# Performance work log

Hardware: AMD Instinct MI355X
Metric: run time of the kernel (lower is better)

## Reference

```python
import jax, jax.numpy as jnp
import numpy as np

N_NODES = 100000
N_EDGES = 1600000
IN_F, HID_F, OUT_F = 64, 64, 64


def setup_inputs() -> dict:
    key = jax.random.key(0)
    ks = jax.random.split(key, 9)
    return {
        "x": jax.random.normal(ks[0], (N_NODES, IN_F), dtype=jnp.float32),
        "src": jax.random.randint(ks[1], (N_EDGES,), 0, N_NODES, dtype=jnp.int64),
        "dst": jax.random.randint(ks[2], (N_EDGES,), 0, N_NODES, dtype=jnp.int64),
        "W_self1": jax.random.normal(ks[3], (IN_F, HID_F), dtype=jnp.float32) * (1.0 / np.sqrt(IN_F)),
        "W_neigh1": jax.random.normal(ks[4], (IN_F, HID_F), dtype=jnp.float32) * (1.0 / np.sqrt(IN_F)),
        "b1": jnp.zeros((HID_F,), dtype=jnp.float32),
        "W_self2": jax.random.normal(ks[5], (HID_F, OUT_F), dtype=jnp.float32) * (1.0 / np.sqrt(HID_F)),
        "W_neigh2": jax.random.normal(ks[6], (HID_F, OUT_F), dtype=jnp.float32) * (1.0 / np.sqrt(HID_F)),
        "b2": jnp.zeros((OUT_F,), dtype=jnp.float32),
    }


def reference(x, src, dst, W_self1, W_neigh1, b1, W_self2, W_neigh2, b2):
    N = x.shape[0]
    # in-degree per destination node; zero-in-degree nodes get zero aggregate (DGL semantics)
    deg = jax.ops.segment_sum(jnp.ones(dst.shape, dtype=x.dtype), dst, num_segments=N)
    inv_deg = jnp.where(deg > 0, 1.0 / jnp.maximum(deg, 1.0), 0.0)[:, None]  # [N,1]

    def sage_conv(h, W_s, W_n, b):
        # mean over in-neighbors: gather src feats, segment-sum at dst, normalize
        agg = jax.ops.segment_sum(h[src], dst, num_segments=N) * inv_deg  # [N,F]
        return h @ W_s + agg @ W_n + b

    h = jax.nn.relu(sage_conv(x, W_self1, W_neigh1, b1))
    return sage_conv(h, W_self2, W_neigh2, b2)
```

## Files before the change

### kernel.cpp

```cpp
#include <hip/hip_runtime.h>

#define N_NODES 100000
#define N_EDGES 1600000
#define NBKT 392
#define BKT_SHIFT 8
#define BKT_MASK 255
#define DL_SHIFT 17
#define SRC_MASK 0x1FFFF
#define NT_TILES 6250
#define CNT_BLOCKS 256
#define CVT_BLOCKS 6250

typedef __attribute__((ext_vector_type(8))) short short8;
typedef __attribute__((ext_vector_type(4))) float float4v;

__device__ __forceinline__ unsigned short f2bf(float f) {
  unsigned u = __float_as_uint(f);
  return (unsigned short)((u + 0x7fffu + ((u >> 16) & 1u)) >> 16);
}
__device__ __forceinline__ float bflo(unsigned d) { return __uint_as_float(d << 16); }
__device__ __forceinline__ float bfhi(unsigned d) { return __uint_as_float(d & 0xffff0000u); }

__device__ __forceinline__ void acc_add(float a[8], uint4 v) {
  a[0] += bflo(v.x); a[1] += bfhi(v.x);
  a[2] += bflo(v.y); a[3] += bfhi(v.y);
  a[4] += bflo(v.z); a[5] += bfhi(v.z);
  a[6] += bflo(v.w); a[7] += bfhi(v.w);
}
__device__ __forceinline__ void acc_fma(float a[8], uint4 v, float m) {
  a[0] = fmaf(m, bflo(v.x), a[0]); a[1] = fmaf(m, bfhi(v.x), a[1]);
  a[2] = fmaf(m, bflo(v.y), a[2]); a[3] = fmaf(m, bfhi(v.y), a[3]);
  a[4] = fmaf(m, bflo(v.z), a[4]); a[5] = fmaf(m, bfhi(v.z), a[5]);
  a[6] = fmaf(m, bflo(v.w), a[6]); a[7] = fmaf(m, bfhi(v.w), a[7]);
}


__global__ void k_prep_count(const float* __restrict__ in, unsigned short* __restrict__ outb,
                             const float* __restrict__ W0, const float* __restrict__ W1,
                             const float* __restrict__ W2, const float* __restrict__ W3,
                             unsigned short* __restrict__ F,
                             const int* __restrict__ dst, int* __restrict__ blkCnt) {
  __shared__ int hist[NBKT];
  const int bid = blockIdx.x;
  if (bid < CNT_BLOCKS) {
    for (int t = threadIdx.x; t < NBKT; t += 256) hist[t] = 0;
    __syncthreads();
    const int e0 = bid * (N_EDGES / CNT_BLOCKS);
    const int e1 = e0 + (N_EDGES / CNT_BLOCKS);
    for (int e = e0 + threadIdx.x; e < e1; e += 256)
      atomicAdd(&hist[dst[e] >> BKT_SHIFT], 1);
    __syncthreads();
    for (int t = threadIdx.x; t < NBKT; t += 256)
      blkCnt[t * CNT_BLOCKS + bid] = hist[t];
    return;
  }
  if (bid < CNT_BLOCKS + 4) {
    if (threadIdx.x >= 64) return;
    const int wsel = bid - CNT_BLOCKS;
    const float* W = (wsel == 0) ? W0 : (wsel == 1) ? W1 : (wsel == 2) ? W2 : W3;
    unsigned short* out = F + wsel * 4096;
    int lane = threadIdx.x;
    int col = lane & 15, kr = lane >> 4;
    #pragma unroll
    for (int kc = 0; kc < 2; kc++)
      #pragma unroll
      for (int nt = 0; nt < 4; nt++) {
        unsigned d[4];
        #pragma unroll
        for (int jj = 0; jj < 4; jj++) {
          float w0 = W[(kc * 32 + kr * 8 + 2 * jj)     * 64 + nt * 16 + col];
          float w1 = W[(kc * 32 + kr * 8 + 2 * jj + 1) * 64 + nt * 16 + col];
          d[jj] = ((unsigned)f2bf(w1) << 16) | f2bf(w0);
        }
        uint4* p = (uint4*)(out + ((kc * 4 + nt) * 64 + lane) * 8);
        *p = make_uint4(d[0], d[1], d[2], d[3]);
      }
    return;
  }
  int i = (bid - CNT_BLOCKS - 4) * 256 + threadIdx.x;
  float4 v = ((const float4*)in)[i];
  unsigned d0 = ((unsigned)f2bf(v.y) << 16) | f2bf(v.x);
  unsigned d1 = ((unsigned)f2bf(v.w) << 16) | f2bf(v.z);
  ((uint2*)outb)[i] = make_uint2(d0, d1);
}


__global__ void kA_scan1(int* __restrict__ blkCnt, int* __restrict__ bktTot) {
  const int b = blockIdx.x;
  const int tid = threadIdx.x, lane = tid & 63, w = tid >> 6;
  int v = blkCnt[b * CNT_BLOCKS + tid];
  int inc = v;
  #pragma unroll
  for (int d = 1; d < 64; d <<= 1) { int y = __shfl_up(inc, d); if (lane >= d) inc += y; }
  __shared__ int wtot[4];
  if (lane == 63) wtot[w] = inc;
  __syncthreads();
  int base = 0;
  for (int j = 0; j < w; j++) base += wtot[j];
  blkCnt[b * CNT_BLOCKS + tid] = base + inc - v;
  if (tid == CNT_BLOCKS - 1) bktTot[b] = base + inc;
}


__global__ void kA_scatter(const int* __restrict__ src, const int* __restrict__ dst,
                           const int* __restrict__ blkCnt, const int* __restrict__ bktTot,
                           int* __restrict__ bktStart, int* __restrict__ binned) {
  __shared__ int ps[NBKT];
  __shared__ int curb[NBKT];
  const int tid = threadIdx.x;
  if (tid < 64) {
    int running = 0;
    for (int base = 0; base < NBKT; base += 64) {
      int i = base + tid;
      int v = (i < NBKT) ? bktTot[i] : 0;
      int inc = v;
      #pragma unroll
      for (int d = 1; d < 64; d <<= 1) { int y = __shfl_up(inc, d); if (tid >= d) inc += y; }
      if (i < NBKT) ps[i] = running + inc - v;
      running += __shfl(inc, 63);
    }
  }
  __syncthreads();
  for (int t = tid; t < NBKT; t += 256)
    curb[t] = ps[t] + blkCnt[t * CNT_BLOCKS + blockIdx.x];
  if (blockIdx.x == 0)
    for (int t = tid; t < NBKT; t += 256) bktStart[t] = ps[t];
  __syncthreads();
  const int e0 = blockIdx.x * (N_EDGES / CNT_BLOCKS);
  const int e1 = e0 + (N_EDGES / CNT_BLOCKS);
  for (int e = e0 + tid; e < e1; e += 256) {
    int d = dst[e];
    int s = src[e];
    int b = d >> BKT_SHIFT;
    int p = atomicAdd(&curb[b], 1);
    binned[p] = s | ((d & BKT_MASK) << DL_SHIFT);
  }
}


__global__ __launch_bounds__(512)
void k_sort(const int* __restrict__ binned, const int* __restrict__ bktStart,
            const int* __restrict__ bktTot,
            int* __restrict__ off, int* __restrict__ esrc) {
  const int b = blockIdx.x;
  const int tid = threadIdx.x, lane = tid & 63, w = tid >> 6;
  __shared__ int cnt[256];
  __shared__ int pos[256];
  __shared__ int wtot[4];
  if (tid < 256) cnt[tid] = 0;
  __syncthreads();
  const int s0 = bktStart[b], ne = bktTot[b];
  for (int i = tid; i < ne; i += 512)
    atomicAdd(&cnt[binned[s0 + i] >> DL_SHIFT], 1);
  __syncthreads();
  if (tid < 256) {
    int c = cnt[tid];
    int inc = c;
    #pragma unroll
    for (int d = 1; d < 64; d <<= 1) { int y = __shfl_up(inc, d); if (lane >= d) inc += y; }
    if (lane == 63) wtot[w] = inc;
    __syncthreads();
    int base = s0;
    for (int j = 0; j < w; j++) base += wtot[j];
    int ex = base + inc - c;
    pos[tid] = ex;
    int n0 = (b << BKT_SHIFT) + tid;
    if (n0 < N_NODES) off[n0] = ex;
    if (n0 == N_NODES - 1) off[N_NODES] = N_EDGES;
  } else {
    __syncthreads();
  }
  __syncthreads();
  for (int i = tid; i < ne; i += 512) {
    int pe = binned[s0 + i];
    int p = atomicAdd(&pos[pe >> DL_SHIFT], 1);
    esrc[p] = pe & SRC_MASK;
  }
}


template <bool RELU, bool OUT_BF>
__global__ void k_fused(const unsigned short* __restrict__ featb,
                        const int* __restrict__ off, const int* __restrict__ esrc,
                        const unsigned short* __restrict__ wfS,
                        const unsigned short* __restrict__ wfN,
                        const float* __restrict__ bias,
                        float* __restrict__ outf, unsigned short* __restrict__ outb) {
  __shared__ unsigned short aggl[4][16 * 64];
  const int tid = threadIdx.x;
  const int lane = tid & 63;
  const int wslot = tid >> 6;
  const int t = (blockIdx.x * blockDim.x + tid) >> 6;
  if (t >= NT_TILES) return;

  unsigned short* lw = &aggl[wslot][0];
  const int n = lane >> 3;
  const int h = lane & 7;

  #pragma unroll
  for (int half = 0; half < 2; ++half) {
    const int row = half * 8 + n;
    const int node = t * 16 + row;
    const int o0 = off[node];
    const int o1 = off[node + 1];
    float a[8];
    #pragma unroll
    for (int q = 0; q < 8; q++) a[q] = 0.f;

    int i = o0;
    for (; i + 8 <= o1; i += 8) {
      int s0 = esrc[i],     s1 = esrc[i + 1], s2 = esrc[i + 2], s3 = esrc[i + 3];
      int s4 = esrc[i + 4], s5 = esrc[i + 5], s6 = esrc[i + 6], s7 = esrc[i + 7];
      uint4 v0 = *(const uint4*)(featb + s0 * 64 + h * 8);
      uint4 v1 = *(const uint4*)(featb + s1 * 64 + h * 8);
      uint4 v2 = *(const uint4*)(featb + s2 * 64 + h * 8);
      uint4 v3 = *(const uint4*)(featb + s3 * 64 + h * 8);
      uint4 v4 = *(const uint4*)(featb + s4 * 64 + h * 8);
      uint4 v5 = *(const uint4*)(featb + s5 * 64 + h * 8);
      uint4 v6 = *(const uint4*)(featb + s6 * 64 + h * 8);
      uint4 v7 = *(const uint4*)(featb + s7 * 64 + h * 8);
      acc_add(a, v0); acc_add(a, v1); acc_add(a, v2); acc_add(a, v3);
      acc_add(a, v4); acc_add(a, v5); acc_add(a, v6); acc_add(a, v7);
    }
    if (i + 4 <= o1) {
      int s0 = esrc[i], s1 = esrc[i + 1], s2 = esrc[i + 2], s3 = esrc[i + 3];
      uint4 v0 = *(const uint4*)(featb + s0 * 64 + h * 8);
      uint4 v1 = *(const uint4*)(featb + s1 * 64 + h * 8);
      uint4 v2 = *(const uint4*)(featb + s2 * 64 + h * 8);
      uint4 v3 = *(const uint4*)(featb + s3 * 64 + h * 8);
      acc_add(a, v0); acc_add(a, v1); acc_add(a, v2); acc_add(a, v3);
      i += 4;
    }
    if (i < o1) {
      int last = o1 - 1;
      int e1 = min(i + 1, last), e2 = min(i + 2, last);
      float m1 = (i + 1 < o1) ? 1.f : 0.f;
      float m2 = (i + 2 < o1) ? 1.f : 0.f;
      int s0 = esrc[i], s1 = esrc[e1], s2 = esrc[e2];
      uint4 v0 = *(const uint4*)(featb + s0 * 64 + h * 8);
      uint4 v1 = *(const uint4*)(featb + s1 * 64 + h * 8);
      uint4 v2 = *(const uint4*)(featb + s2 * 64 + h * 8);
      acc_add(a, v0); acc_fma(a, v1, m1); acc_fma(a, v2, m2);
    }

    const int dg = o1 - o0;
    const float inv = (dg > 0) ? (1.0f / (float)dg) : 0.f;
    unsigned d0 = ((unsigned)f2bf(a[1] * inv) << 16) | f2bf(a[0] * inv);
    unsigned d1 = ((unsigned)f2bf(a[3] * inv) << 16) | f2bf(a[2] * inv);
    unsigned d2 = ((unsigned)f2bf(a[5] * inv) << 16) | f2bf(a[4] * inv);
    unsigned d3 = ((unsigned)f2bf(a[7] * inv) << 16) | f2bf(a[6] * inv);
    *(uint4*)(lw + row * 64 + ((h ^ (row & 7)) << 3)) = make_uint4(d0, d1, d2, d3);
  }

  __builtin_amdgcn_wave_barrier();
  asm volatile("" ::: "memory");

  const int col = lane & 15, rr = lane >> 4;
  const int m = t * 16 + col;
  short8 as0 = *(const short8*)(featb + m * 64 + rr * 8);
  short8 as1 = *(const short8*)(featb + m * 64 + 32 + rr * 8);
  short8 aa0 = *(const short8*)(lw + col * 64 + ((rr ^ (col & 7)) << 3));
  short8 aa1 = *(const short8*)(lw + col * 64 + (((rr + 4) ^ (col & 7)) << 3));

  #pragma unroll
  for (int nt = 0; nt < 4; nt++) {
    short8 bs0 = *(const short8*)(wfS + ((0 * 4 + nt) * 64 + lane) * 8);
    short8 bs1 = *(const short8*)(wfS + ((1 * 4 + nt) * 64 + lane) * 8);
    short8 bn0 = *(const short8*)(wfN + ((0 * 4 + nt) * 64 + lane) * 8);
    short8 bn1 = *(const short8*)(wfN + ((1 * 4 + nt) * 64 + lane) * 8);
    float bvn = bias[nt * 16 + col];
    float4v cfr = {bvn, bvn, bvn, bvn};
    cfr = __builtin_amdgcn_mfma_f32_16x16x32_bf16(as0, bs0, cfr, 0, 0, 0);
    cfr = __builtin_amdgcn_mfma_f32_16x16x32_bf16(as1, bs1, cfr, 0, 0, 0);
    cfr = __builtin_amdgcn_mfma_f32_16x16x32_bf16(aa0, bn0, cfr, 0, 0, 0);
    cfr = __builtin_amdgcn_mfma_f32_16x16x32_bf16(aa1, bn1, cfr, 0, 0, 0);
    #pragma unroll
    for (int r2 = 0; r2 < 4; r2++) {
      int row = t * 16 + rr * 4 + r2;
      float v = cfr[r2];
      if (RELU) v = fmaxf(v, 0.f);
      if (OUT_BF) outb[row * 64 + nt * 16 + col] = f2bf(v);
      else        outf[row * 64 + nt * 16 + col] = v;
    }
  }
}


extern "C" void kernel_launch(void* const* d_in, const int* in_sizes, int n_in,
                              void* d_out, int out_size, void* d_ws, size_t ws_size,
                              hipStream_t stream) {
  const float* x   = (const float*)d_in[0];
  const int*   src = (const int*)d_in[1];
  const int*   dst = (const int*)d_in[2];
  const float* Ws1 = (const float*)d_in[3];
  const float* Wn1 = (const float*)d_in[4];
  const float* b1  = (const float*)d_in[5];
  const float* Ws2 = (const float*)d_in[6];
  const float* Wn2 = (const float*)d_in[7];
  const float* b2  = (const float*)d_in[8];

  char* ws = (char*)d_ws;
  int*            blkCnt   = (int*)(ws + 0);
  int*            bktTot   = (int*)(ws + 401408);
  int*            bktStart = (int*)(ws + 403008);
  unsigned short* wf       = (unsigned short*)(ws + 404608);
  int*            off      = (int*)(ws + 437376);
  int*            binned   = (int*)(ws + 837440);
  int*            esrc     = (int*)(ws + 7237440);
  unsigned short* xbf      = (unsigned short*)(ws + 13637440);
  unsigned short* hbf      = (unsigned short*)(ws + 26437440);

  k_prep_count<<<CNT_BLOCKS + 4 + CVT_BLOCKS, 256, 0, stream>>>(
      x, xbf, Ws1, Wn1, Ws2, Wn2, wf, dst, blkCnt);
  kA_scan1<<<NBKT, 256, 0, stream>>>(blkCnt, bktTot);
  kA_scatter<<<CNT_BLOCKS, 256, 0, stream>>>(src, dst, blkCnt, bktTot, bktStart, binned);
  k_sort<<<NBKT, 512, 0, stream>>>(binned, bktStart, bktTot, off, esrc);

  k_fused<true, true><<<1563, 256, 0, stream>>>(xbf, off, esrc, wf + 0 * 4096,
                                                wf + 1 * 4096, b1, nullptr, hbf);
  k_fused<false, false><<<1563, 256, 0, stream>>>(hbf, off, esrc, wf + 2 * 4096,
                                                  wf + 3 * 4096, b2, (float*)d_out, nullptr);
}
```

Before: 238.8 us.

## Fuse bucket scan into scatter and CSR sort into first SAGE layer

Removes the separate scan and sort kernels. Each scatter block now recomputes the bucket totals and its own prefix from the count matrix, and the first layer's fused kernel builds its per-bucket CSR in LDS and aggregates from there, while also writing off/esrc for layer two. Buckets shrink to 128 nodes, and the bf16 conversion now does four elements per thread. This cuts launches and global round trips of the edge lists, at the cost of redundant per-block row sums. It also caps per-bucket edges at ESRC_CAP, which assumes a fairly uniform in-degree distribution.

After: 217.6 us. 8.9% less time.

```diff
diff --git a/kernel.cpp b/kernel.cpp
--- a/kernel.cpp
+++ b/kernel.cpp
@@ -2,14 +2,16 @@
 
 #define N_NODES 100000
 #define N_EDGES 1600000
-#define NBKT 392
-#define BKT_SHIFT 8
-#define BKT_MASK 255
+#define BKT 128
+#define NBKT 782
+#define BKT_SHIFT 7
+#define BKT_MASK 127
 #define DL_SHIFT 17
 #define SRC_MASK 0x1FFFF
 #define NT_TILES 6250
-#define CNT_BLOCKS 256
-#define CVT_BLOCKS 6250
+#define CNT_BLOCKS 128
+#define CVT_BLOCKS 1563
+#define ESRC_CAP 3072
 
 typedef __attribute__((ext_vector_type(8))) short short8;
 typedef __attribute__((ext_vector_type(4))) float float4v;
@@ -77,42 +79,47 @@
       }
     return;
   }
-  int i = (bid - CNT_BLOCKS - 4) * 256 + threadIdx.x;
-  float4 v = ((const float4*)in)[i];
-  unsigned d0 = ((unsigned)f2bf(v.y) << 16) | f2bf(v.x);
-  unsigned d1 = ((unsigned)f2bf(v.w) << 16) | f2bf(v.z);
-  ((uint2*)outb)[i] = make_uint2(d0, d1);
-}
-
-
-__global__ void kA_scan1(int* __restrict__ blkCnt, int* __restrict__ bktTot) {
-  const int b = blockIdx.x;
-  const int tid = threadIdx.x, lane = tid & 63, w = tid >> 6;
-  int v = blkCnt[b * CNT_BLOCKS + tid];
-  int inc = v;
-  #pragma unroll
-  for (int d = 1; d < 64; d <<= 1) { int y = __shfl_up(inc, d); if (lane >= d) inc += y; }
-  __shared__ int wtot[4];
-  if (lane == 63) wtot[w] = inc;
-  __syncthreads();
-  int base = 0;
-  for (int j = 0; j < w; j++) base += wtot[j];
-  blkCnt[b * CNT_BLOCKS + tid] = base + inc - v;
-  if (tid == CNT_BLOCKS - 1) bktTot[b] = base + inc;
-}
-
-
-__global__ void kA_scatter(const int* __restrict__ src, const int* __restrict__ dst,
-                           const int* __restrict__ blkCnt, const int* __restrict__ bktTot,
-                           int* __restrict__ bktStart, int* __restrict__ binned) {
+  const int base = (bid - CNT_BLOCKS - 4) * 1024 + threadIdx.x;
+  #pragma unroll
+  for (int j = 0; j < 4; j++) {
+    int i = base + j * 256;
+    if (i < 1600000) {
+      float4 v = ((const float4*)in)[i];
+      unsigned d0 = ((unsigned)f2bf(v.y) << 16) | f2bf(v.x);
+      unsigned d1 = ((unsigned)f2bf(v.w) << 16) | f2bf(v.z);
+      ((uint2*)outb)[i] = make_uint2(d0, d1);
+    }
+  }
+}
+
+
+__global__ __launch_bounds__(512)
+void k_scatter(const int* __restrict__ src, const int* __restrict__ dst,
+               const int* __restrict__ blkCnt, int* __restrict__ bktStart,
+               int* __restrict__ bktTot, int* __restrict__ binned) {
+  __shared__ int totsh[NBKT];
   __shared__ int ps[NBKT];
   __shared__ int curb[NBKT];
   const int tid = threadIdx.x;
+  const int bid = blockIdx.x;
+  for (int t = tid; t < NBKT; t += 512) {
+    const int* row = blkCnt + t * CNT_BLOCKS;
+    int tot = 0, part = 0;
+    #pragma unroll 4
+    for (int i = 0; i < CNT_BLOCKS; i++) {
+      int v = row[i];
+      tot += v;
+      if (i < bid) part += v;
+    }
+    totsh[t] = tot;
+    curb[t] = part;
+  }
+  __syncthreads();
   if (tid < 64) {
     int running = 0;
     for (int base = 0; base < NBKT; base += 64) {
       int i = base + tid;
-      int v = (i < NBKT) ? bktTot[i] : 0;
+      int v = (i < NBKT) ? totsh[i] : 0;
       int inc = v;
       #pragma unroll
       for (int d = 1; d < 64; d <<= 1) { int y = __shfl_up(inc, d); if (tid >= d) inc += y; }
@@ -121,129 +128,104 @@
     }
   }
   __syncthreads();
-  for (int t = tid; t < NBKT; t += 256)
-    curb[t] = ps[t] + blkCnt[t * CNT_BLOCKS + blockIdx.x];
-  if (blockIdx.x == 0)
-    for (int t = tid; t < NBKT; t += 256) bktStart[t] = ps[t];
-  __syncthreads();
-  const int e0 = blockIdx.x * (N_EDGES / CNT_BLOCKS);
+  for (int t = tid; t < NBKT; t += 512) curb[t] += ps[t];
+  if (bid == 0)
+    for (int t = tid; t < NBKT; t += 512) { bktStart[t] = ps[t]; bktTot[t] = totsh[t]; }
+  __syncthreads();
+  const int e0 = bid * (N_EDGES / CNT_BLOCKS);
   const int e1 = e0 + (N_EDGES / CNT_BLOCKS);
-  for (int e = e0 + tid; e < e1; e += 256) {
+  for (int e = e0 + tid; e < e1; e += 512) {
     int d = dst[e];
     int s = src[e];
-    int b = d >> BKT_SHIFT;
-    int p = atomicAdd(&curb[b], 1);
+    int p = atomicAdd(&curb[d >> BKT_SHIFT], 1);
     binned[p] = s | ((d & BKT_MASK) << DL_SHIFT);
   }
 }
 
 
 __global__ __launch_bounds__(512)
-void k_sort(const int* __restrict__ binned, const int* __restrict__ bktStart,
-            const int* __restrict__ bktTot,
-            int* __restrict__ off, int* __restrict__ esrc) {
+void k_fused1(const unsigned short* __restrict__ featb, const int* __restrict__ binned,
+              const int* __restrict__ bktStart, const int* __restrict__ bktTot,
+              const unsigned short* __restrict__ wfS, const unsigned short* __restrict__ wfN,
+              const float* __restrict__ bias,
+              unsigned short* __restrict__ outb,
+              int* __restrict__ off, int* __restrict__ esrc) {
+  __shared__ int cnt[BKT];
+  __shared__ int st[BKT];
+  __shared__ int pos[BKT];
+  __shared__ int wtot[2];
+  __shared__ int esrc_l[ESRC_CAP];
+  __shared__ unsigned short aggl[8][16 * 64];
   const int b = blockIdx.x;
-  const int tid = threadIdx.x, lane = tid & 63, w = tid >> 6;
-  __shared__ int cnt[256];
-  __shared__ int pos[256];
-  __shared__ int wtot[4];
-  if (tid < 256) cnt[tid] = 0;
+  const int tid = threadIdx.x, lane = tid & 63;
+  const int wv = tid >> 6;
+
+  if (tid < BKT) cnt[tid] = 0;
   __syncthreads();
   const int s0 = bktStart[b], ne = bktTot[b];
   for (int i = tid; i < ne; i += 512)
     atomicAdd(&cnt[binned[s0 + i] >> DL_SHIFT], 1);
   __syncthreads();
-  if (tid < 256) {
-    int c = cnt[tid];
-    int inc = c;
+  int c = 0, inc = 0;
+  if (tid < BKT) {
+    c = cnt[tid]; inc = c;
     #pragma unroll
     for (int d = 1; d < 64; d <<= 1) { int y = __shfl_up(inc, d); if (lane >= d) inc += y; }
-    if (lane == 63) wtot[w] = inc;
-    __syncthreads();
-    int base = s0;
-    for (int j = 0; j < w; j++) base += wtot[j];
-    int ex = base + inc - c;
-    pos[tid] = ex;
+    if (lane == 63) wtot[tid >> 6] = inc;
+  }
+  __syncthreads();
+  if (tid < BKT) {
+    int ex = inc - c + ((tid >= 64) ? wtot[0] : 0);
+    st[tid] = ex; pos[tid] = ex;
     int n0 = (b << BKT_SHIFT) + tid;
-    if (n0 < N_NODES) off[n0] = ex;
+    if (n0 < N_NODES) off[n0] = s0 + ex;
     if (n0 == N_NODES - 1) off[N_NODES] = N_EDGES;
-  } else {
-    __syncthreads();
   }
   __syncthreads();
   for (int i = tid; i < ne; i += 512) {
     int pe = binned[s0 + i];
     int p = atomicAdd(&pos[pe >> DL_SHIFT], 1);
-    esrc[p] = pe & SRC_MASK;
-  }
-}
-
-
-template <bool RELU, bool OUT_BF>
-__global__ void k_fused(const unsigned short* __restrict__ featb,
-                        const int* __restrict__ off, const int* __restrict__ esrc,
-                        const unsigned short* __restrict__ wfS,
-                        const unsigned short* __restrict__ wfN,
-                        const float* __restrict__ bias,
-                        float* __restrict__ outf, unsigned short* __restrict__ outb) {
-  __shared__ unsigned short aggl[4][16 * 64];
-  const int tid = threadIdx.x;
-  const int lane = tid & 63;
-  const int wslot = tid >> 6;
-  const int t = (blockIdx.x * blockDim.x + tid) >> 6;
-  if (t >= NT_TILES) return;
-
-  unsigned short* lw = &aggl[wslot][0];
+    if (p < ESRC_CAP) esrc_l[p] = pe & SRC_MASK;
+  }
+  __syncthreads();
+  for (int i = tid; i < ne; i += 512) esrc[s0 + i] = esrc_l[i];
+
+  unsigned short* lw = &aggl[wv][0];
   const int n = lane >> 3;
   const int h = lane & 7;
 
   #pragma unroll
   for (int half = 0; half < 2; ++half) {
     const int row = half * 8 + n;
-    const int node = t * 16 + row;
-    const int o0 = off[node];
-    const int o1 = off[node + 1];
+    const int lnode = wv * 16 + row;
+    const int o0 = st[lnode];
+    const int dg = cnt[lnode];
+    const int o1 = o0 + dg;
     float a[8];
     #pragma unroll
     for (int q = 0; q < 8; q++) a[q] = 0.f;
 
     int i = o0;
-    for (; i + 8 <= o1; i += 8) {
-      int s0 = esrc[i],     s1 = esrc[i + 1], s2 = esrc[i + 2], s3 = esrc[i + 3];
-      int s4 = esrc[i + 4], s5 = esrc[i + 5], s6 = esrc[i + 6], s7 = esrc[i + 7];
-      uint4 v0 = *(const uint4*)(featb + s0 * 64 + h * 8);
-      uint4 v1 = *(const uint4*)(featb + s1 * 64 + h * 8);
-      uint4 v2 = *(const uint4*)(featb + s2 * 64 + h * 8);
-      uint4 v3 = *(const uint4*)(featb + s3 * 64 + h * 8);
-      uint4 v4 = *(const uint4*)(featb + s4 * 64 + h * 8);
-      uint4 v5 = *(const uint4*)(featb + s5 * 64 + h * 8);
-      uint4 v6 = *(const uint4*)(featb + s6 * 64 + h * 8);
-      uint4 v7 = *(const uint4*)(featb + s7 * 64 + h * 8);
+    for (; i + 4 <= o1; i += 4) {
+      int s0e = esrc_l[i], s1e = esrc_l[i + 1], s2e = esrc_l[i + 2], s3e = esrc_l[i + 3];
+      uint4 v0 = *(const uint4*)(featb + s0e * 64 + h * 8);
+      uint4 v1 = *(const uint4*)(featb + s1e * 64 + h * 8);
+      uint4 v2 = *(const uint4*)(featb + s2e * 64 + h * 8);
+      uint4 v3 = *(const uint4*)(featb + s3e * 64 + h * 8);
       acc_add(a, v0); acc_add(a, v1); acc_add(a, v2); acc_add(a, v3);
-      acc_add(a, v4); acc_add(a, v5); acc_add(a, v6); acc_add(a, v7);
-    }
-    if (i + 4 <= o1) {
-      int s0 = esrc[i], s1 = esrc[i + 1], s2 = esrc[i + 2], s3 = esrc[i + 3];
-      uint4 v0 = *(const uint4*)(featb + s0 * 64 + h * 8);
-      uint4 v1 = *(const uint4*)(featb + s1 * 64 + h * 8);
-      uint4 v2 = *(const uint4*)(featb + s2 * 64 + h * 8);
-      uint4 v3 = *(const uint4*)(featb + s3 * 64 + h * 8);
-      acc_add(a, v0); acc_add(a, v1); acc_add(a, v2); acc_add(a, v3);
-      i += 4;
     }
     if (i < o1) {
       int last = o1 - 1;
       int e1 = min(i + 1, last), e2 = min(i + 2, last);
       float m1 = (i + 1 < o1) ? 1.f : 0.f;
       float m2 = (i + 2 < o1) ? 1.f : 0.f;
-      int s0 = esrc[i], s1 = esrc[e1], s2 = esrc[e2];
-      uint4 v0 = *(const uint4*)(featb + s0 * 64 + h * 8);
-      uint4 v1 = *(const uint4*)(featb + s1 * 64 + h * 8);
-      uint4 v2 = *(const uint4*)(featb + s2 * 64 + h * 8);
+      int s0e = esrc_l[i], s1e = esrc_l[e1], s2e = esrc_l[e2];
+      uint4 v0 = *(const uint4*)(featb + s0e * 64 + h * 8);
+      uint4 v1 = *(const uint4*)(featb + s1e * 64 + h * 8);
+      uint4 v2 = *(const uint4*)(featb + s2e * 64 + h * 8);
       acc_add(a, v0); acc_fma(a, v1, m1); acc_fma(a, v2, m2);
     }
 
-    const int dg = o1 - o0;
     const float inv = (dg > 0) ? (1.0f / (float)dg) : 0.f;
     unsigned d0 = ((unsigned)f2bf(a[1] * inv) << 16) | f2bf(a[0] * inv);
     unsigned d1 = ((unsigned)f2bf(a[3] * inv) << 16) | f2bf(a[2] * inv);
@@ -255,8 +237,10 @@
   __builtin_amdgcn_wave_barrier();
   asm volatile("" ::: "memory");
 
+  const int tbase = (b << BKT_SHIFT) + wv * 16;
+  if (tbase >= N_NODES) return;
   const int col = lane & 15, rr = lane >> 4;
-  const int m = t * 16 + col;
+  const int m = tbase + col;
   short8 as0 = *(const short8*)(featb + m * 64 + rr * 8);
   short8 as1 = *(const short8*)(featb + m * 64 + 32 + rr * 8);
   short8 aa0 = *(const short8*)(lw + col * 64 + ((rr ^ (col & 7)) << 3));
@@ -276,11 +260,96 @@
     cfr = __builtin_amdgcn_mfma_f32_16x16x32_bf16(aa1, bn1, cfr, 0, 0, 0);
     #pragma unroll
     for (int r2 = 0; r2 < 4; r2++) {
+      int row = tbase + rr * 4 + r2;
+      float v = fmaxf(cfr[r2], 0.f);
+      outb[row * 64 + nt * 16 + col] = f2bf(v);
+    }
+  }
+}
+
+
+__global__ void k_fused2(const unsigned short* __restrict__ featb,
+                         const int* __restrict__ off, const int* __restrict__ esrc,
+                         const unsigned short* __restrict__ wfS,
+                         const unsigned short* __restrict__ wfN,
+                         const float* __restrict__ bias, float* __restrict__ outf) {
+  __shared__ unsigned short aggl[4][16 * 64];
+  const int tid = threadIdx.x;
+  const int lane = tid & 63;
+  const int wslot = tid >> 6;
+  const int t = (blockIdx.x * blockDim.x + tid) >> 6;
+  if (t >= NT_TILES) return;
+
+  unsigned short* lw = &aggl[wslot][0];
+  const int n = lane >> 3;
+  const int h = lane & 7;
+
+  #pragma unroll
+  for (int half = 0; half < 2; ++half) {
+    const int row = half * 8 + n;
+    const int node = t * 16 + row;
+    const int o0 = off[node];
+    const int o1 = off[node + 1];
+    float a[8];
+    #pragma unroll
+    for (int q = 0; q < 8; q++) a[q] = 0.f;
+
+    int i = o0;
+    for (; i + 4 <= o1; i += 4) {
+      int s0 = esrc[i], s1 = esrc[i + 1], s2 = esrc[i + 2], s3 = esrc[i + 3];
+      uint4 v0 = *(const uint4*)(featb + s0 * 64 + h * 8);
+      uint4 v1 = *(const uint4*)(featb + s1 * 64 + h * 8);
+      uint4 v2 = *(const uint4*)(featb + s2 * 64 + h * 8);
+      uint4 v3 = *(const uint4*)(featb + s3 * 64 + h * 8);
+      acc_add(a, v0); acc_add(a, v1); acc_add(a, v2); acc_add(a, v3);
+    }
+    if (i < o1) {
+      int last = o1 - 1;
+      int e1 = min(i + 1, last), e2 = min(i + 2, last);
+      float m1 = (i + 1 < o1) ? 1.f : 0.f;
+      float m2 = (i + 2 < o1) ? 1.f : 0.f;
+      int s0 = esrc[i], s1 = esrc[e1], s2 = esrc[e2];
+      uint4 v0 = *(const uint4*)(featb + s0 * 64 + h * 8);
+      uint4 v1 = *(const uint4*)(featb + s1 * 64 + h * 8);
+      uint4 v2 = *(const uint4*)(featb + s2 * 64 + h * 8);
+      acc_add(a, v0); acc_fma(a, v1, m1); acc_fma(a, v2, m2);
+    }
+
+    const int dg = o1 - o0;
+    const float inv = (dg > 0) ? (1.0f / (float)dg) : 0.f;
+    unsigned d0 = ((unsigned)f2bf(a[1] * inv) << 16) | f2bf(a[0] * inv);
+    unsigned d1 = ((unsigned)f2bf(a[3] * inv) << 16) | f2bf(a[2] * inv);
+    unsigned d2 = ((unsigned)f2bf(a[5] * inv) << 16) | f2bf(a[4] * inv);
+    unsigned d3 = ((unsigned)f2bf(a[7] * inv) << 16) | f2bf(a[6] * inv);
+    *(uint4*)(lw + row * 64 + ((h ^ (row & 7)) << 3)) = make_uint4(d0, d1, d2, d3);
+  }
+
+  __builtin_amdgcn_wave_barrier();
+  asm volatile("" ::: "memory");
+
+  const int col = lane & 15, rr = lane >> 4;
+  const int m = t * 16 + col;
+  short8 as0 = *(const short8*)(featb + m * 64 + rr * 8);
+  short8 as1 = *(const short8*)(featb + m * 64 + 32 + rr * 8);
+  short8 aa0 = *(const short8*)(lw + col * 64 + ((rr ^ (col & 7)) << 3));
+  short8 aa1 = *(const short8*)(lw + col * 64 + (((rr + 4) ^ (col & 7)) << 3));
+
+  #pragma unroll
+  for (int nt = 0; nt < 4; nt++) {
+    short8 bs0 = *(const short8*)(wfS + ((0 * 4 + nt) * 64 + lane) * 8);
+    short8 bs1 = *(const short8*)(wfS + ((1 * 4 + nt) * 64 + lane) * 8);
+    short8 bn0 = *(const short8*)(wfN + ((0 * 4 + nt) * 64 + lane) * 8);
+    short8 bn1 = *(const short8*)(wfN + ((1 * 4 + nt) * 64 + lane) * 8);
+    float bvn = bias[nt * 16 + col];
+    float4v cfr = {bvn, bvn, bvn, bvn};
+    cfr = __builtin_amdgcn_mfma_f32_16x16x32_bf16(as0, bs0, cfr, 0, 0, 0);
+    cfr = __builtin_amdgcn_mfma_f32_16x16x32_bf16(as1, bs1, cfr, 0, 0, 0);
+    cfr = __builtin_amdgcn_mfma_f32_16x16x32_bf16(aa0, bn0, cfr, 0, 0, 0);
+    cfr = __builtin_amdgcn_mfma_f32_16x16x32_bf16(aa1, bn1, cfr, 0, 0, 0);
+    #pragma unroll
+    for (int r2 = 0; r2 < 4; r2++) {
       int row = t * 16 + rr * 4 + r2;
-      float v = cfr[r2];
-      if (RELU) v = fmaxf(v, 0.f);
-      if (OUT_BF) outb[row * 64 + nt * 16 + col] = f2bf(v);
-      else        outf[row * 64 + nt * 16 + col] = v;
+      outf[row * 64 + nt * 16 + col] = cfr[r2];
     }
   }
 }
@@ -301,23 +370,21 @@
 
   char* ws = (char*)d_ws;
   int*            blkCnt   = (int*)(ws + 0);
-  int*            bktTot   = (int*)(ws + 401408);
-  int*            bktStart = (int*)(ws + 403008);
-  unsigned short* wf       = (unsigned short*)(ws + 404608);
-  int*            off      = (int*)(ws + 437376);
-  int*            binned   = (int*)(ws + 837440);
-  int*            esrc     = (int*)(ws + 7237440);
-  unsigned short* xbf      = (unsigned short*)(ws + 13637440);
-  unsigned short* hbf      = (unsigned short*)(ws + 26437440);
+  int*            bktTot   = (int*)(ws + 400384);
+  int*            bktStart = (int*)(ws + 403512);
+  unsigned short* wf       = (unsigned short*)(ws + 406656);
+  int*            off      = (int*)(ws + 439424);
+  int*            binned   = (int*)(ws + 839680);
+  int*            esrc     = (int*)(ws + 7239680);
+  unsigned short* xbf      = (unsigned short*)(ws + 13639680);
+  unsigned short* hbf      = (unsigned short*)(ws + 26439680);
 
   k_prep_count<<<CNT_BLOCKS + 4 + CVT_BLOCKS, 256, 0, stream>>>(
       x, xbf, Ws1, Wn1, Ws2, Wn2, wf, dst, blkCnt);
-  kA_scan1<<<NBKT, 256, 0, stream>>>(blkCnt, bktTot);
-  kA_scatter<<<CNT_BLOCKS, 256, 0, stream>>>(src, dst, blkCnt, bktTot, bktStart, binned);
-  k_sort<<<NBKT, 512, 0, stream>>>(binned, bktStart, bktTot, off, esrc);
-
-  k_fused<true, true><<<1563, 256, 0, stream>>>(xbf, off, esrc, wf + 0 * 4096,
-                                                wf + 1 * 4096, b1, nullptr, hbf);
-  k_fused<false, false><<<1563, 256, 0, stream>>>(hbf, off, esrc, wf + 2 * 4096,
-                                                  wf + 3 * 4096, b2, (float*)d_out, nullptr);
-}
+  k_scatter<<<CNT_BLOCKS, 512, 0, stream>>>(src, dst, blkCnt, bktStart, bktTot, binned);
+
+  k_fused1<<<NBKT, 512, 0, stream>>>(xbf, binned, bktStart, bktTot,
+                                     wf + 0 * 4096, wf + 1 * 4096, b1, hbf, off, esrc);
+  k_fused2<<<1563, 256, 0, stream>>>(hbf, off, esrc, wf + 2 * 4096, wf + 3 * 4096,
+                                     b2, (float*)d_out);
+}
```

## Widen sort buckets, batch bf16 conversion, and software-pipeline edge index loads

Applied to the files above, without the earlier changes.

Bucket width for the edge sort doubles to 512 nodes, so there are half as many buckets and each sort block uses all 512 threads in its scan. The fp32-to-bf16 conversion now handles four float4s per thread, which cuts the conversion block count. The aggregation loop prefetches the next four source indices while the current feature gathers are in flight, and the remainder path reuses those prefetched indices. The esrc buffer is padded with four zeros so the prefetch can read past the end safely. Fewer, larger sort blocks may balance load less evenly.

Result: faster. 200.1 us (median of 2 runs) (-16.2%).

```diff
diff --git a/kernel.cpp b/kernel.cpp
--- a/kernel.cpp
+++ b/kernel.cpp
@@ -2,14 +2,14 @@
 
 #define N_NODES 100000
 #define N_EDGES 1600000
-#define NBKT 392
-#define BKT_SHIFT 8
-#define BKT_MASK 255
+#define NBKT 196
+#define BKT_SHIFT 9
+#define BKT_MASK 511
 #define DL_SHIFT 17
 #define SRC_MASK 0x1FFFF
 #define NT_TILES 6250
 #define CNT_BLOCKS 256
-#define CVT_BLOCKS 6250
+#define CVT_BLOCKS 1563
 
 typedef __attribute__((ext_vector_type(8))) short short8;
 typedef __attribute__((ext_vector_type(4))) float float4v;
@@ -77,11 +77,17 @@
       }
     return;
   }
-  int i = (bid - CNT_BLOCKS - 4) * 256 + threadIdx.x;
-  float4 v = ((const float4*)in)[i];
-  unsigned d0 = ((unsigned)f2bf(v.y) << 16) | f2bf(v.x);
-  unsigned d1 = ((unsigned)f2bf(v.w) << 16) | f2bf(v.z);
-  ((uint2*)outb)[i] = make_uint2(d0, d1);
+  const int base = (bid - CNT_BLOCKS - 4) * 1024 + threadIdx.x;
+  #pragma unroll
+  for (int j = 0; j < 4; j++) {
+    int i = base + j * 256;
+    if (i < 1600000) {
+      float4 v = ((const float4*)in)[i];
+      unsigned d0 = ((unsigned)f2bf(v.y) << 16) | f2bf(v.x);
+      unsigned d1 = ((unsigned)f2bf(v.w) << 16) | f2bf(v.z);
+      ((uint2*)outb)[i] = make_uint2(d0, d1);
+    }
+  }
 }
 
 
@@ -144,32 +150,29 @@
             int* __restrict__ off, int* __restrict__ esrc) {
   const int b = blockIdx.x;
   const int tid = threadIdx.x, lane = tid & 63, w = tid >> 6;
-  __shared__ int cnt[256];
-  __shared__ int pos[256];
-  __shared__ int wtot[4];
-  if (tid < 256) cnt[tid] = 0;
+  __shared__ int cnt[512];
+  __shared__ int pos[512];
+  __shared__ int wtot[8];
+  cnt[tid] = 0;
   __syncthreads();
   const int s0 = bktStart[b], ne = bktTot[b];
   for (int i = tid; i < ne; i += 512)
     atomicAdd(&cnt[binned[s0 + i] >> DL_SHIFT], 1);
   __syncthreads();
-  if (tid < 256) {
-    int c = cnt[tid];
-    int inc = c;
-    #pragma unroll
-    for (int d = 1; d < 64; d <<= 1) { int y = __shfl_up(inc, d); if (lane >= d) inc += y; }
-    if (lane == 63) wtot[w] = inc;
-    __syncthreads();
-    int base = s0;
-    for (int j = 0; j < w; j++) base += wtot[j];
-    int ex = base + inc - c;
-    pos[tid] = ex;
-    int n0 = (b << BKT_SHIFT) + tid;
-    if (n0 < N_NODES) off[n0] = ex;
-    if (n0 == N_NODES - 1) off[N_NODES] = N_EDGES;
-  } else {
-    __syncthreads();
-  }
+  int c = cnt[tid];
+  int inc = c;
+  #pragma unroll
+  for (int d = 1; d < 64; d <<= 1) { int y = __shfl_up(inc, d); if (lane >= d) inc += y; }
+  if (lane == 63) wtot[w] = inc;
+  __syncthreads();
+  int base = s0;
+  for (int j = 0; j < w; j++) base += wtot[j];
+  int ex = base + inc - c;
+  pos[tid] = ex;
+  int n0 = (b << BKT_SHIFT) + tid;
+  if (n0 < N_NODES) off[n0] = ex;
+  if (b == NBKT - 1 && tid == 0) off[N_NODES] = N_EDGES;
+  if (b == NBKT - 1 && tid < 4) esrc[N_EDGES + tid] = 0;
   __syncthreads();
   for (int i = tid; i < ne; i += 512) {
     int pe = binned[s0 + i];
@@ -208,38 +211,25 @@
     for (int q = 0; q < 8; q++) a[q] = 0.f;
 
     int i = o0;
-    for (; i + 8 <= o1; i += 8) {
-      int s0 = esrc[i],     s1 = esrc[i + 1], s2 = esrc[i + 2], s3 = esrc[i + 3];
-      int s4 = esrc[i + 4], s5 = esrc[i + 5], s6 = esrc[i + 6], s7 = esrc[i + 7];
-      uint4 v0 = *(const uint4*)(featb + s0 * 64 + h * 8);
-      uint4 v1 = *(const uint4*)(featb + s1 * 64 + h * 8);
-      uint4 v2 = *(const uint4*)(featb + s2 * 64 + h * 8);
-      uint4 v3 = *(const uint4*)(featb + s3 * 64 + h * 8);
-      uint4 v4 = *(const uint4*)(featb + s4 * 64 + h * 8);
-      uint4 v5 = *(const uint4*)(featb + s5 * 64 + h * 8);
-      uint4 v6 = *(const uint4*)(featb + s6 * 64 + h * 8);
-      uint4 v7 = *(const uint4*)(featb + s7 * 64 + h * 8);
+    int s0e = esrc[i], s1e = esrc[i + 1], s2e = esrc[i + 2], s3e = esrc[i + 3];
+    for (; i + 4 <= o1; ) {
+      uint4 v0 = *(const uint4*)(featb + s0e * 64 + h * 8);
+      uint4 v1 = *(const uint4*)(featb + s1e * 64 + h * 8);
+      uint4 v2 = *(const uint4*)(featb + s2e * 64 + h * 8);
+      uint4 v3 = *(const uint4*)(featb + s3e * 64 + h * 8);
+      i += 4;
+      s0e = esrc[i]; s1e = esrc[i + 1]; s2e = esrc[i + 2]; s3e = esrc[i + 3];
       acc_add(a, v0); acc_add(a, v1); acc_add(a, v2); acc_add(a, v3);
-      acc_add(a, v4); acc_add(a, v5); acc_add(a, v6); acc_add(a, v7);
-    }
-    if (i + 4 <= o1) {
-      int s0 = esrc[i], s1 = esrc[i + 1], s2 = esrc[i + 2], s3 = esrc[i + 3];
-      uint4 v0 = *(const uint4*)(featb + s0 * 64 + h * 8);
-      uint4 v1 = *(const uint4*)(featb + s1 * 64 + h * 8);
-      uint4 v2 = *(const uint4*)(featb + s2 * 64 + h * 8);
-      uint4 v3 = *(const uint4*)(featb + s3 * 64 + h * 8);
-      acc_add(a, v0); acc_add(a, v1); acc_add(a, v2); acc_add(a, v3);
-      i += 4;
     }
     if (i < o1) {
-      int last = o1 - 1;
-      int e1 = min(i + 1, last), e2 = min(i + 2, last);
-      float m1 = (i + 1 < o1) ? 1.f : 0.f;
-      float m2 = (i + 2 < o1) ? 1.f : 0.f;
-      int s0 = esrc[i], s1 = esrc[e1], s2 = esrc[e2];
-      uint4 v0 = *(const uint4*)(featb + s0 * 64 + h * 8);
-      uint4 v1 = *(const uint4*)(featb + s1 * 64 + h * 8);
-      uint4 v2 = *(const uint4*)(featb + s2 * 64 + h * 8);
+      const int rem = o1 - i;
+      int t1 = (rem > 1) ? s1e : s0e;
+      int t2 = (rem > 2) ? s2e : s0e;
+      float m1 = (rem > 1) ? 1.f : 0.f;
+      float m2 = (rem > 2) ? 1.f : 0.f;
+      uint4 v0 = *(const uint4*)(featb + s0e * 64 + h * 8);
+      uint4 v1 = *(const uint4*)(featb + t1 * 64 + h * 8);
+      uint4 v2 = *(const uint4*)(featb + t2 * 64 + h * 8);
       acc_add(a, v0); acc_fma(a, v1, m1); acc_fma(a, v2, m2);
     }
 
@@ -301,18 +291,18 @@
 
   char* ws = (char*)d_ws;
   int*            blkCnt   = (int*)(ws + 0);
-  int*            bktTot   = (int*)(ws + 401408);
-  int*            bktStart = (int*)(ws + 403008);
-  unsigned short* wf       = (unsigned short*)(ws + 404608);
-  int*            off      = (int*)(ws + 437376);
-  int*            binned   = (int*)(ws + 837440);
-  int*            esrc     = (int*)(ws + 7237440);
-  unsigned short* xbf      = (unsigned short*)(ws + 13637440);
-  unsigned short* hbf      = (unsigned short*)(ws + 26437440);
+  int*            bktTot   = (int*)(ws + 200704);
+  int*            bktStart = (int*)(ws + 201488);
+  unsigned short* wf       = (unsigned short*)(ws + 202272);
+  int*            off      = (int*)(ws + 235040);
+  int*            binned   = (int*)(ws + 635072);
+  int*            esrc     = (int*)(ws + 7035072);
+  unsigned short* xbf      = (unsigned short*)(ws + 13435136);
+  unsigned short* hbf      = (unsigned short*)(ws + 26235136);
 
   k_prep_count<<<CNT_BLOCKS + 4 + CVT_BLOCKS, 256, 0, stream>>>(
       x, xbf, Ws1, Wn1, Ws2, Wn2, wf, dst, blkCnt);
-  kA_scan1<<<NBKT, 256, 0, stream>>>(blkCnt, bktTot);
+  kA_scan1<<<NBKT, CNT_BLOCKS, 0, stream>>>(blkCnt, bktTot);
   kA_scatter<<<CNT_BLOCKS, 256, 0, stream>>>(src, dst, blkCnt, bktTot, bktStart, binned);
   k_sort<<<NBKT, 512, 0, stream>>>(binned, bktStart, bktTot, off, esrc);
 
```
